# Kernel optimization log

Hardware: AMD Instinct MI355X
Metric: run time of the kernel (lower is better)

## Reference

```python
import jax, jax.numpy as jnp
import numpy as np

B, T, D, N = 4, 1024, 1024, 16
DH = D // N
INF = 1.0e10
SCALE = float(np.sqrt(D))  # module scales by sqrt(d_key) == sqrt(D), NOT sqrt(d_head)


def setup_inputs() -> dict:
    key = jax.random.key(0)
    ks = jax.random.split(key, 10)
    stdv = 1.0 / np.sqrt(D)
    inp = {
        "query": jax.random.normal(ks[0], (B, T, D), jnp.float32),
        "key": jax.random.normal(ks[1], (B, T, D), jnp.float32),
        "value": jax.random.normal(ks[2], (B, T, D), jnp.float32),
        "mask": jnp.ones((B, T), jnp.float32),
        "weights": jax.random.normal(ks[3], (B * N, T, T), jnp.float32) * 0.1,
        "Wq": jax.random.uniform(ks[4], (D, D), jnp.float32, -stdv, stdv),
        "bq": jnp.zeros((D,), jnp.float32),
        "Wk": jax.random.uniform(ks[5], (D, D), jnp.float32, -stdv, stdv),
        "bk": jnp.zeros((D,), jnp.float32),
        "Wv": jax.random.uniform(ks[6], (D, D), jnp.float32, -stdv, stdv),
        "bv": jnp.zeros((D,), jnp.float32),
        "Wo": jax.random.uniform(ks[7], (D, D), jnp.float32, -stdv, stdv),
        "bo": jnp.zeros((D,), jnp.float32),
    }
    return inp


def reference(query, key, value, mask, weights, Wq, bq, Wk, bk, Wv, bv, Wo, bo):
    # projections then split heads: [B,T,D] -> [B,N,T,DH]
    q = (query @ Wq.T + bq).reshape(B, T, N, DH).transpose(0, 2, 1, 3)
    k = (key @ Wk.T + bk).reshape(B, T, N, DH).transpose(0, 2, 1, 3)
    v = (value @ Wv.T + bv).reshape(B, T, N, DH).transpose(0, 2, 1, 3)

    dot = jnp.einsum("bnqd,bnkd->bnqk", q, k)            # [B,N,T,T]
    dot = dot + weights.reshape(B, N, T, T)               # additive external bias
    tri = jnp.triu(jnp.full((T, T), INF, dot.dtype), 1)   # causal: subtract INF above diag
    dot = dot - tri[None, None, :, :]
    dot = dot - (1.0 - mask)[:, None, None, :] * INF      # key padding mask

    probs = jax.nn.softmax(dot / SCALE, axis=-1)
    out = jnp.einsum("bnqk,bnkd->bnqd", probs, v)         # [B,N,T,DH]
    out = out.transpose(0, 2, 1, 3).reshape(B, T, D)      # merge heads
    return out @ Wo.T + bo
```

## Files before the change

### kernel.cpp

```cpp
#include <hip/hip_runtime.h>
#include <cstddef>


typedef __attribute__((ext_vector_type(8))) short bf16x8;
typedef __attribute__((ext_vector_type(4))) float f32x4;

#define MFMA16(a, b, c) __builtin_amdgcn_mfma_f32_16x16x32_bf16(a, b, c, 0, 0, 0)

__device__ __forceinline__ short f2bf(float f) {
  union { float f; unsigned int i; } v; v.f = f;
  unsigned int r = v.i + 0x7FFFu + ((v.i >> 16) & 1u);
  return (short)(r >> 16);
}

__device__ __forceinline__ float fast_exp2(float x) {
  float r;
  asm volatile("v_exp_f32 %0, %1" : "=v"(r) : "v"(x));
  return r;
}

__device__ __forceinline__ unsigned int cvt_pk_bf16(float lo, float hi) {
  unsigned int r;
  asm volatile("v_cvt_pk_bf16_f32 %0, %1, %2" : "=v"(r) : "v"(lo), "v"(hi));
  return r;
}

__device__ __forceinline__ void gload_lds16(const void* g, void* l) {
  __builtin_amdgcn_global_load_lds(
      (const __attribute__((address_space(1))) void*)g,
      (__attribute__((address_space(3))) void*)l, 16, 0, 0);
}

__global__ __launch_bounds__(256) void cvt_all(
    const float* __restrict__ q, const float* __restrict__ k, const float* __restrict__ v,
    const float* __restrict__ wq, const float* __restrict__ wk,
    const float* __restrict__ wv, const float* __restrict__ wo,
    short* __restrict__ qb, short* __restrict__ kb, short* __restrict__ vb,
    short* __restrict__ wqb, short* __restrict__ wkb,
    short* __restrict__ wvb, short* __restrict__ wob) {
  const int total = 16 * 1048576 / 4;
  int stride = gridDim.x * blockDim.x;
  for (int i = blockIdx.x * blockDim.x + threadIdx.x; i < total; i += stride) {
    int e = i * 4;
    int chunk = e >> 20;
    const float* s;
    short* d;
    int off;
    if (chunk < 12) {
      if (chunk < 4)      { s = q; d = qb; }
      else if (chunk < 8) { s = k; d = kb; }
      else                { s = v; d = vb; }
      off = e & (4 * 1048576 - 1);
    } else {
      int w = chunk - 12;
      if (w == 0)      { s = wq; d = wqb; }
      else if (w == 1) { s = wk; d = wkb; }
      else if (w == 2) { s = wv; d = wvb; }
      else             { s = wo; d = wob; }
      off = e & (1048576 - 1);
    }
    float4 x = *(const float4*)(s + off);
    short4 o;
    o.x = f2bf(x.x); o.y = f2bf(x.y); o.z = f2bf(x.z); o.w = f2bf(x.w);
    *(short4*)(d + off) = o;
  }
}

__global__ __launch_bounds__(256) void proj_qkv(
    const short* __restrict__ qA, const short* __restrict__ kA, const short* __restrict__ vA,
    const short* __restrict__ Wqb, const short* __restrict__ Wkb, const short* __restrict__ Wvb,
    const float* __restrict__ bq, const float* __restrict__ bk, const float* __restrict__ bv,
    short* __restrict__ Qh, short* __restrict__ Kh, short* __restrict__ Vth) {
  __shared__ short DS[2][16384];

  const int m0 = blockIdx.x * 128;
  const int n0 = blockIdx.y * 128;
  const int z = blockIdx.z;

  const short *A, *W;
  const float* bias;
  if (z == 0)      { A = qA; W = Wqb; bias = bq; }
  else if (z == 1) { A = kA; W = Wkb; bias = bk; }
  else             { A = vA; W = Wvb; bias = bv; }

  const int tid = threadIdx.x;
  const int wid = tid >> 6, lane = tid & 63;
  const int wr = wid >> 1, wc = wid & 1;
  const int fr = lane & 15, fq = lane >> 4;

  auto stage = [&](int buf, int kt) {
#pragma unroll
    for (int c = 0; c < 4; ++c) {
      int pbase = c * 4096 + wid * 1024;
      int pb = pbase + lane * 16;
      int lb = pb ^ (((pb >> 7) & 7) << 4);
      int grow = lb >> 7, gcol = (lb & 127) >> 1;
      gload_lds16(A + (size_t)(m0 + grow) * 1024 + kt * 64 + gcol,
                  (char*)DS[buf] + pbase);
      gload_lds16(W + (size_t)(n0 + grow) * 1024 + kt * 64 + gcol,
                  (char*)(DS[buf] + 8192) + pbase);
    }
  };

  f32x4 acc[4][4] = {};
  stage(0, 0);
  __syncthreads();
  int cur = 0;

  for (int kt = 0; kt < 16; ++kt) {
    if (kt < 15) stage(cur ^ 1, kt + 1);
    const short* As = DS[cur];
    const short* Bs = DS[cur] + 8192;
#pragma unroll
    for (int kk = 0; kk < 2; ++kk) {
      bf16x8 af[4], bg[4];
      int cb = (fq * 8 + kk * 32) * 2;
#pragma unroll
      for (int m = 0; m < 4; ++m) {
        int r = wr * 64 + m * 16 + fr;
        af[m] = *(const bf16x8*)((const char*)As + (((r << 7) + cb) ^ ((r & 7) << 4)));
      }
#pragma unroll
      for (int n = 0; n < 4; ++n) {
        int r = wc * 64 + n * 16 + fr;
        bg[n] = *(const bf16x8*)((const char*)Bs + (((r << 7) + cb) ^ ((r & 7) << 4)));
      }
#pragma unroll
      for (int m = 0; m < 4; ++m)
#pragma unroll
        for (int n = 0; n < 4; ++n)
          acc[m][n] = MFMA16(af[m], bg[n], acc[m][n]);
    }
    __syncthreads();
    cur ^= 1;
  }

  const int bb = m0 >> 10, t0 = m0 & 1023;
  if (z < 2) {
    short* Tt = (short*)DS;
    short* dst = (z == 0) ? Qh : Kh;
#pragma unroll
    for (int m = 0; m < 4; ++m)
#pragma unroll
      for (int n = 0; n < 4; ++n) {
        int coll = wc * 64 + n * 16 + fr;
        float bval = bias[n0 + coll];
        int rowl0 = wr * 64 + m * 16 + fq * 4;
#pragma unroll
        for (int j = 0; j < 4; ++j)
          Tt[(rowl0 + j) * 136 + coll] = f2bf(acc[m][n][j] + bval);
      }
    __syncthreads();
#pragma unroll
    for (int it = 0; it < 8; ++it) {
      int qq = tid + it * 256;
      int rowl = qq >> 4, seg = qq & 15;
      bf16x8 vv = *(const bf16x8*)&Tt[rowl * 136 + seg * 8];
      int col = n0 + seg * 8;
      int hh = col >> 6, dh = col & 63;
      *(bf16x8*)&dst[(((size_t)(bb * 16 + hh)) * 1024 + t0 + rowl) * 64 + dh] = vv;
    }
  } else {
    short* Vt = (short*)DS;
#pragma unroll
    for (int m = 0; m < 4; ++m)
#pragma unroll
      for (int n = 0; n < 4; ++n) {
        int coll = wc * 64 + n * 16 + fr;
        float bval = bias[n0 + coll];
        int rowl0 = wr * 64 + m * 16 + fq * 4;
#pragma unroll
        for (int j = 0; j < 4; ++j)
          Vt[coll * 136 + rowl0 + j] = f2bf(acc[m][n][j] + bval);
      }
    __syncthreads();
#pragma unroll
    for (int it = 0; it < 8; ++it) {
      int qq = tid + it * 256;
      int rowl = qq >> 4, seg = qq & 15;
      bf16x8 vv = *(const bf16x8*)&Vt[rowl * 136 + seg * 8];
      int cg = n0 + rowl, hh = cg >> 6, dh = cg & 63;
      *(bf16x8*)&Vth[(((size_t)(bb * 16 + hh)) * 64 + dh) * 1024 + t0 + seg * 8] = vv;
    }
  }
}

__global__ __launch_bounds__(512) void gemm_out(const short* __restrict__ A,
                                                const short* __restrict__ W,
                                                const float* __restrict__ bias,
                                                float* __restrict__ C) {
  __shared__ short DS[2][16384];

  const int m0 = blockIdx.x * 128;
  const int n0 = blockIdx.y * 128;

  const int tid = threadIdx.x;
  const int wid = tid >> 6, lane = tid & 63;
  const int wr = wid >> 2, wc = wid & 3;
  const int fr = lane & 15, fq = lane >> 4;

  auto stage = [&](int buf, int kt) {
#pragma unroll
    for (int c = 0; c < 2; ++c) {
      int pbase = c * 8192 + wid * 1024;
      int pb = pbase + lane * 16;
      int lb = pb ^ (((pb >> 7) & 7) << 4);
      int grow = lb >> 7, gcol = (lb & 127) >> 1;
      gload_lds16(A + (size_t)(m0 + grow) * 1024 + kt * 64 + gcol,
                  (char*)DS[buf] + pbase);
      gload_lds16(W + (size_t)(n0 + grow) * 1024 + kt * 64 + gcol,
                  (char*)(DS[buf] + 8192) + pbase);
    }
  };

  f32x4 acc[4][2] = {};
  stage(0, 0);
  __syncthreads();
  int cur = 0;

  for (int kt = 0; kt < 16; ++kt) {
    if (kt < 15) stage(cur ^ 1, kt + 1);
    const short* As = DS[cur];
    const short* Bs = DS[cur] + 8192;
#pragma unroll
    for (int kk = 0; kk < 2; ++kk) {
      bf16x8 af[4], bg[2];
      int cb = (fq * 8 + kk * 32) * 2;
#pragma unroll
      for (int m = 0; m < 4; ++m) {
        int r = wr * 64 + m * 16 + fr;
        af[m] = *(const bf16x8*)((const char*)As + (((r << 7) + cb) ^ ((r & 7) << 4)));
      }
#pragma unroll
      for (int n = 0; n < 2; ++n) {
        int r = wc * 32 + n * 16 + fr;
        bg[n] = *(const bf16x8*)((const char*)Bs + (((r << 7) + cb) ^ ((r & 7) << 4)));
      }
#pragma unroll
      for (int m = 0; m < 4; ++m)
#pragma unroll
        for (int n = 0; n < 2; ++n)
          acc[m][n] = MFMA16(af[m], bg[n], acc[m][n]);
    }
    __syncthreads();
    cur ^= 1;
  }

#pragma unroll
  for (int m = 0; m < 4; ++m)
#pragma unroll
    for (int n = 0; n < 2; ++n) {
      int col = n0 + wc * 32 + n * 16 + fr;
      float bval = bias[col];
      int row0 = m0 + wr * 64 + m * 16 + fq * 4;
#pragma unroll
      for (int j = 0; j < 4; ++j)
        C[(size_t)(row0 + j) * 1024 + col] = acc[m][n][j] + bval;
    }
}

__global__ __launch_bounds__(256) void attn_kernel(
    const short* __restrict__ Qh, const short* __restrict__ Kh,
    const short* __restrict__ Vth, const float* __restrict__ Wb,
    const float* __restrict__ mask, short* __restrict__ Aout) {
  __shared__ short Ks[2][4096];
  __shared__ short Vs[2][4096];
  __shared__ float Bi[2][4096];
  __shared__ unsigned short Mp[1024];
  __shared__ short Ps[4][16 * 72];

  const int tid = threadIdx.x;
  const int wid = tid >> 6, lane = tid & 63;
  const int fr = lane & 15, fq = lane >> 4;
  const int h = blockIdx.y, b = h >> 4;
  const int bx = blockIdx.x;

  const float C2 = 0.045084439f;
  const float PEN2 = 4.5084440e8f;

  const short* Kbase = Kh + (size_t)h * 1024 * 64;
  const short* Vbase = Vth + (size_t)h * 64 * 1024;
  const float* wbase = Wb + (size_t)h * 1024 * 1024;

  auto stage = [&](int buf, int kt2, int q0) {
    const int k0 = kt2 * 64;
#pragma unroll
    for (int c = 0; c < 2; ++c) {
      int pbase = c * 4096 + wid * 1024;
      int pb = pbase + lane * 16;
      int lb = pb ^ (((pb >> 7) & 7) << 4);
      int grow = lb >> 7, gcol = (lb & 127) >> 1;
      gload_lds16(Kbase + (size_t)(k0 + grow) * 64 + gcol, (char*)Ks[buf] + pbase);
      gload_lds16(Vbase + (size_t)grow * 1024 + k0 + gcol, (char*)Vs[buf] + pbase);
    }
#pragma unroll
    for (int c = 0; c < 4; ++c) {
      int pbase = c * 4096 + wid * 1024;
      int pb = pbase + lane * 16;
      int lb = pb ^ (((pb >> 8) & 7) << 4);
      int grow = lb >> 8, gcolf = (lb & 255) >> 2;
      gload_lds16(wbase + (size_t)(q0 + grow) * 1024 + k0 + gcolf,
                  (char*)Bi[buf] + pbase);
    }
  };

  {
    float4 mv = *(const float4*)(mask + b * 1024 + tid * 4);
    ushort4 mp;
    mp.x = (unsigned short)f2bf((1.0f - mv.x) * PEN2);
    mp.y = (unsigned short)f2bf((1.0f - mv.y) * PEN2);
    mp.z = (unsigned short)f2bf((1.0f - mv.z) * PEN2);
    mp.w = (unsigned short)f2bf((1.0f - mv.w) * PEN2);
    *(ushort4*)&Mp[tid * 4] = mp;
  }

  for (int half = 0; half < 2; ++half) {
    const int qi = half ? bx : 15 - bx;
    const int q0 = qi * 64;
    const int qrow = q0 + wid * 16 + fr;
    const int NT = qi + 1;

    const short* qbase = Qh + ((size_t)h * 1024 + qrow) * 64 + fq * 8;
    bf16x8 qf0 = *(const bf16x8*)qbase;
    bf16x8 qf1 = *(const bf16x8*)(qbase + 32);

    if (half) {
      __builtin_amdgcn_sched_barrier(0);
      __builtin_amdgcn_s_barrier();
      __builtin_amdgcn_sched_barrier(0);
    }
    stage(0, 0, q0);
    if (NT > 1) stage(1, 1, q0);
    if (NT > 1) asm volatile("s_waitcnt vmcnt(8) lgkmcnt(0)" ::: "memory");
    else        asm volatile("s_waitcnt vmcnt(0) lgkmcnt(0)" ::: "memory");
    __builtin_amdgcn_sched_barrier(0);
    __builtin_amdgcn_s_barrier();
    __builtin_amdgcn_sched_barrier(0);

    f32x4 o_acc[4] = {};
    float m_run = -3.0e38f, l_run = 0.f;
    int cur = 0;

    for (int kt = 0; kt < NT; ++kt) {
      const int k0 = kt * 64;
      const bool diag = (kt == NT - 1);

      f32x4 s_acc[4] = {};
      __builtin_amdgcn_s_setprio(1);
#pragma unroll
      for (int kk = 0; kk < 2; ++kk)
#pragma unroll
        for (int nt = 0; nt < 4; ++nt) {
          int r = nt * 16 + fr;
          int cb = fq * 16 + kk * 64;
          bf16x8 kf = *(const bf16x8*)((const char*)Ks[cur] + (((r << 7) + cb) ^ ((r & 7) << 4)));
          s_acc[nt] = MFMA16(kf, kk == 0 ? qf0 : qf1, s_acc[nt]);
        }
      __builtin_amdgcn_s_setprio(0);

      f32x4 bv[4];
#pragma unroll
      for (int nt = 0; nt < 4; ++nt) {
        int lbyte = (wid * 16 + fr) * 256 + nt * 64 + fq * 16;
        bv[nt] = *(const f32x4*)((const char*)Bi[cur] + (lbyte ^ ((fr & 7) << 4)));
      }
      float pen[16];
#pragma unroll
      for (int nt = 0; nt < 4; ++nt) {
        ushort4 m4 = *(const ushort4*)&Mp[k0 + nt * 16 + fq * 4];
        pen[nt * 4 + 0] = __uint_as_float((unsigned)m4.x << 16);
        pen[nt * 4 + 1] = __uint_as_float((unsigned)m4.y << 16);
        pen[nt * 4 + 2] = __uint_as_float((unsigned)m4.z << 16);
        pen[nt * 4 + 3] = __uint_as_float((unsigned)m4.w << 16);
      }

      float p[16];
#pragma unroll
      for (int nt = 0; nt < 4; ++nt)
#pragma unroll
        for (int j = 0; j < 4; ++j) {
          float s = (s_acc[nt][j] + bv[nt][j]) * C2 - pen[nt * 4 + j];
          if (diag && (nt * 16 + fq * 4 + j) > (wid * 16 + fr)) s = -3.0e38f;
          p[nt * 4 + j] = s;
        }

      float t8[8], t4m[4];
#pragma unroll
      for (int i = 0; i < 8; ++i) t8[i] = fmaxf(p[i], p[i + 8]);
#pragma unroll
      for (int i = 0; i < 4; ++i) t4m[i] = fmaxf(t8[i], t8[i + 4]);
      float pmax = fmaxf(fmaxf(t4m[0], t4m[1]), fmaxf(t4m[2], t4m[3]));
      pmax = fmaxf(pmax, __shfl_xor(pmax, 16));
      pmax = fmaxf(pmax, __shfl_xor(pmax, 32));

      if (!__all(pmax - m_run <= 11.5f)) {
        float mnew = fmaxf(m_run, pmax);
        float corr = fast_exp2(m_run - mnew);
        m_run = mnew;
        l_run *= corr;
#pragma unroll
        for (int nt = 0; nt < 4; ++nt) o_acc[nt] *= corr;
      }

#pragma unroll
      for (int i = 0; i < 16; ++i) p[i] = fast_exp2(p[i] - m_run);
      float a8[8], a4[4];
#pragma unroll
      for (int i = 0; i < 8; ++i) a8[i] = p[i] + p[i + 8];
#pragma unroll
      for (int i = 0; i < 4; ++i) a4[i] = a8[i] + a8[i + 4];
      float rsum = (a4[0] + a4[1]) + (a4[2] + a4[3]);
      rsum += __shfl_xor(rsum, 16);
      rsum += __shfl_xor(rsum, 32);
      l_run += rsum;

#pragma unroll
      for (int nt = 0; nt < 4; ++nt) {
        uint2 w2;
        w2.x = cvt_pk_bf16(p[nt * 4 + 0], p[nt * 4 + 1]);
        w2.y = cvt_pk_bf16(p[nt * 4 + 2], p[nt * 4 + 3]);
        *(uint2*)&Ps[wid][fr * 72 + nt * 16 + fq * 4] = w2;
      }
      asm volatile("s_waitcnt lgkmcnt(0)" ::: "memory");
      __builtin_amdgcn_sched_barrier(0);
      bf16x8 pf0 = *(const bf16x8*)&Ps[wid][fr * 72 + fq * 8];
      bf16x8 pf1 = *(const bf16x8*)&Ps[wid][fr * 72 + fq * 8 + 32];

      __builtin_amdgcn_s_setprio(1);
#pragma unroll
      for (int kk = 0; kk < 2; ++kk)
#pragma unroll
        for (int nt = 0; nt < 4; ++nt) {
          int r = nt * 16 + fr;
          int cb = fq * 16 + kk * 64;
          bf16x8 vf = *(const bf16x8*)((const char*)Vs[cur] + (((r << 7) + cb) ^ ((r & 7) << 4)));
          o_acc[nt] = MFMA16(vf, kk == 0 ? pf0 : pf1, o_acc[nt]);
        }
      __builtin_amdgcn_s_setprio(0);

      if (kt + 2 < NT) {
        __builtin_amdgcn_sched_barrier(0);
        __builtin_amdgcn_s_barrier();
        __builtin_amdgcn_sched_barrier(0);
        stage(cur, kt + 2, q0);
      }
      if (kt + 1 < NT) {
        if (kt + 2 < NT) asm volatile("s_waitcnt vmcnt(8)" ::: "memory");
        else             asm volatile("s_waitcnt vmcnt(0)" ::: "memory");
        __builtin_amdgcn_sched_barrier(0);
        __builtin_amdgcn_s_barrier();
        __builtin_amdgcn_sched_barrier(0);
      }
      cur ^= 1;
    }

    float rl = 1.0f / l_run;
    size_t row = (size_t)(b * 1024 + q0 + wid * 16 + fr);
#pragma unroll
    for (int nt = 0; nt < 4; ++nt) {
      uint2 sv;
      sv.x = cvt_pk_bf16(o_acc[nt][0] * rl, o_acc[nt][1] * rl);
      sv.y = cvt_pk_bf16(o_acc[nt][2] * rl, o_acc[nt][3] * rl);
      int col = (h & 15) * 64 + nt * 16 + fq * 4;
      *(uint2*)&Aout[row * 1024 + col] = sv;
    }
  }
}

extern "C" void kernel_launch(void* const* d_in, const int* in_sizes, int n_in,
                              void* d_out, int out_size, void* d_ws, size_t ws_size,
                              hipStream_t stream) {
  const float* query = (const float*)d_in[0];
  const float* key   = (const float*)d_in[1];
  const float* value = (const float*)d_in[2];
  const float* mask  = (const float*)d_in[3];
  const float* wts   = (const float*)d_in[4];
  const float* Wq    = (const float*)d_in[5];
  const float* bq    = (const float*)d_in[6];
  const float* Wk    = (const float*)d_in[7];
  const float* bk    = (const float*)d_in[8];
  const float* Wv    = (const float*)d_in[9];
  const float* bv    = (const float*)d_in[10];
  const float* Wo    = (const float*)d_in[11];
  const float* bo    = (const float*)d_in[12];

  char* ws = (char*)d_ws;
  const size_t MB = 1u << 20;
  short* qbf = (short*)(ws + 0);
  short* kbf = (short*)(ws + 8 * MB);
  short* vbf = (short*)(ws + 16 * MB);
  short* Wqb = (short*)(ws + 24 * MB);
  short* Wkb = (short*)(ws + 26 * MB);
  short* Wvb = (short*)(ws + 28 * MB);
  short* Wob = (short*)(ws + 30 * MB);
  short* Qh  = (short*)(ws + 32 * MB);
  short* Kh  = (short*)(ws + 40 * MB);
  short* Vth = (short*)(ws + 48 * MB);
  short* attnb = qbf;

  cvt_all<<<dim3(2048), dim3(256), 0, stream>>>(query, key, value, Wq, Wk, Wv, Wo,
                                                qbf, kbf, vbf, Wqb, Wkb, Wvb, Wob);
  proj_qkv<<<dim3(32, 8, 3), dim3(256), 0, stream>>>(qbf, kbf, vbf, Wqb, Wkb, Wvb,
                                                     bq, bk, bv, Qh, Kh, Vth);
  attn_kernel<<<dim3(8, 64), dim3(256), 0, stream>>>(Qh, Kh, Vth, wts, mask, attnb);
  gemm_out<<<dim3(32, 8), dim3(512), 0, stream>>>(attnb, Wob, bo, (float*)d_out);
}
```

Before: 118.3 us.

## Prefetch two K-tiles ahead with partial vmcnt waits in projection GEMMs

After: 111.2 us, median of 2. -6.0%, faster.

```diff
diff --git a/kernel.cpp b/kernel.cpp
--- a/kernel.cpp
+++ b/kernel.cpp
@@ -104,13 +104,15 @@
 
   f32x4 acc[4][4] = {};
   stage(0, 0);
-  __syncthreads();
-  int cur = 0;
+  stage(1, 1);
+  asm volatile("s_waitcnt vmcnt(8)" ::: "memory");
+  __builtin_amdgcn_sched_barrier(0);
+  __builtin_amdgcn_s_barrier();
+  __builtin_amdgcn_sched_barrier(0);
 
   for (int kt = 0; kt < 16; ++kt) {
-    if (kt < 15) stage(cur ^ 1, kt + 1);
-    const short* As = DS[cur];
-    const short* Bs = DS[cur] + 8192;
+    const short* As = DS[kt & 1];
+    const short* Bs = DS[kt & 1] + 8192;
 #pragma unroll
     for (int kk = 0; kk < 2; ++kk) {
       bf16x8 af[4], bg[4];
@@ -131,9 +133,23 @@
         for (int n = 0; n < 4; ++n)
           acc[m][n] = MFMA16(af[m], bg[n], acc[m][n]);
     }
-    __syncthreads();
-    cur ^= 1;
+    if (kt + 2 < 16) {
+      __builtin_amdgcn_sched_barrier(0);
+      __builtin_amdgcn_s_barrier();
+      __builtin_amdgcn_sched_barrier(0);
+      stage(kt & 1, kt + 2);
+    }
+    if (kt + 1 < 16) {
+      if (kt + 2 < 16) asm volatile("s_waitcnt vmcnt(8)" ::: "memory");
+      else             asm volatile("s_waitcnt vmcnt(0)" ::: "memory");
+      __builtin_amdgcn_sched_barrier(0);
+      __builtin_amdgcn_s_barrier();
+      __builtin_amdgcn_sched_barrier(0);
+    }
   }
+  __builtin_amdgcn_sched_barrier(0);
+  __builtin_amdgcn_s_barrier();
+  __builtin_amdgcn_sched_barrier(0);
 
   const int bb = m0 >> 10, t0 = m0 & 1023;
   if (z < 2) {
@@ -215,13 +231,15 @@
 
   f32x4 acc[4][2] = {};
   stage(0, 0);
-  __syncthreads();
-  int cur = 0;
+  stage(1, 1);
+  asm volatile("s_waitcnt vmcnt(4)" ::: "memory");
+  __builtin_amdgcn_sched_barrier(0);
+  __builtin_amdgcn_s_barrier();
+  __builtin_amdgcn_sched_barrier(0);
 
   for (int kt = 0; kt < 16; ++kt) {
-    if (kt < 15) stage(cur ^ 1, kt + 1);
-    const short* As = DS[cur];
-    const short* Bs = DS[cur] + 8192;
+    const short* As = DS[kt & 1];
+    const short* Bs = DS[kt & 1] + 8192;
 #pragma unroll
     for (int kk = 0; kk < 2; ++kk) {
       bf16x8 af[4], bg[2];
@@ -242,8 +260,19 @@
         for (int n = 0; n < 2; ++n)
           acc[m][n] = MFMA16(af[m], bg[n], acc[m][n]);
     }
-    __syncthreads();
-    cur ^= 1;
+    if (kt + 2 < 16) {
+      __builtin_amdgcn_sched_barrier(0);
+      __builtin_amdgcn_s_barrier();
+      __builtin_amdgcn_sched_barrier(0);
+      stage(kt & 1, kt + 2);
+    }
+    if (kt + 1 < 16) {
+      if (kt + 2 < 16) asm volatile("s_waitcnt vmcnt(4)" ::: "memory");
+      else             asm volatile("s_waitcnt vmcnt(0)" ::: "memory");
+      __builtin_amdgcn_sched_barrier(0);
+      __builtin_amdgcn_s_barrier();
+      __builtin_amdgcn_sched_barrier(0);
+    }
   }
 
 #pragma unroll
```
